# Performance work log

Measured on AMD Instinct MI355X. Metric: run time of the kernel, lower is better.

The kernel has to match this reference:

```python
import jax, jax.numpy as jnp
import numpy as np

B, T = 8, 512
ACT, EMB, DET, HID, NST = 32, 1024, 1024, 1024, 16
STO, CLS = 32, 32
UNIMIX = 0.01


def _ln(x, g, b):
    m = x.mean(-1, keepdims=True)
    v = x.var(-1, keepdims=True)
    return (x - m) / jnp.sqrt(v + 1e-5) * g + b


def _lnsilu(x, g, b):
    return jax.nn.silu(_ln(x, g, b))


def setup_inputs() -> dict:
    key = jax.random.key(0)
    ks = iter(jax.random.split(key, 40))

    def lin(din, dout):
        return jax.random.normal(next(ks), (din, dout), jnp.float32) / np.sqrt(din)

    actions = jax.random.normal(next(ks), (B, T, ACT), jnp.float32)
    embeds = jax.random.normal(next(ks), (B, T, EMB), jnp.float32)
    # pre_ssm: Linear(ACT,HID) + LayerNormSiLU(HID)
    W_pre, b_pre = lin(ACT, HID), jnp.zeros(HID)
    g_pre, bb_pre = jnp.ones(HID), jnp.zeros(HID)
    W_emb = lin(EMB, HID)  # bias=False
    W_in, b_in = lin(HID, 2 * DET), jnp.zeros(2 * DET)
    W_dt = lin(DET, DET)
    # dt bias init: inverse-softplus of dt ~ LogUniform(1e-3, 0.1)
    u = jax.random.uniform(next(ks), (DET,), jnp.float32)
    dt_init = jnp.exp(u * (np.log(0.1) - np.log(1e-3)) + np.log(1e-3))
    b_dt = dt_init + jnp.log(-jnp.expm1(-dt_init))
    W_B, W_C = lin(DET, NST), lin(DET, NST)
    A_log = jnp.broadcast_to(
        jnp.log(jnp.arange(1, NST + 1, dtype=jnp.float32)), (DET, NST)
    ) + jnp.zeros((DET, NST))
    Dp = jnp.ones(DET)
    g_out, b_out = jnp.ones(DET), jnp.zeros(DET)
    # prior_net: Linear(DET,HID)+LNSiLU+Linear(HID,STO*CLS)
    W_pr1, b_pr1 = lin(DET, HID), jnp.zeros(HID)
    g_pr, bb_pr = jnp.ones(HID), jnp.zeros(HID)
    W_pr2, b_pr2 = lin(HID, STO * CLS), jnp.zeros(STO * CLS)
    # post_net: Linear(DET+EMB,HID)+LNSiLU+Linear(HID,STO*CLS)
    W_po1, b_po1 = lin(DET + EMB, HID), jnp.zeros(HID)
    g_po, bb_po = jnp.ones(HID), jnp.zeros(HID)
    W_po2, b_po2 = lin(HID, STO * CLS), jnp.zeros(STO * CLS)
    return dict(actions=actions, embeds=embeds, W_pre=W_pre, b_pre=b_pre,
                g_pre=g_pre, bb_pre=bb_pre, W_emb=W_emb, W_in=W_in, b_in=b_in,
                W_dt=W_dt, b_dt=b_dt, W_B=W_B, W_C=W_C, A_log=A_log, Dp=Dp,
                g_out=g_out, b_out=b_out, W_pr1=W_pr1, b_pr1=b_pr1, g_pr=g_pr,
                bb_pr=bb_pr, W_pr2=W_pr2, b_pr2=b_pr2, W_po1=W_po1, b_po1=b_po1,
                g_po=g_po, bb_po=bb_po, W_po2=W_po2, b_po2=b_po2)


def reference(actions, embeds, W_pre, b_pre, g_pre, bb_pre, W_emb, W_in, b_in,
              W_dt, b_dt, W_B, W_C, A_log, Dp, g_out, b_out, W_pr1, b_pr1,
              g_pr, bb_pr, W_pr2, b_pr2, W_po1, b_po1, g_po, bb_po, W_po2, b_po2):
    # input projections
    x = _lnsilu(actions @ W_pre + b_pre, g_pre, bb_pre) + embeds @ W_emb  # (B,T,HID)
    x = x.transpose(1, 0, 2)  # (T,B,HID)
    xz = x @ W_in + b_in
    x_ssm, x_gate = xz[..., :DET], xz[..., DET:]
    dt = jax.nn.softplus(x_ssm @ W_dt + b_dt)        # (T,B,DET)
    Bp = x_ssm @ W_B                                  # (T,B,NST)
    Cp = x_ssm @ W_C                                  # (T,B,NST)
    A = -jnp.exp(A_log)                               # (DET,NST)
    gates = jnp.exp(dt[..., None] * A)                # (T,B,DET,NST)
    values = (dt * x_ssm)[..., None] * Bp[:, :, None, :]

    # linear recurrence h[t] = g[t]*h[t-1] + v[t] via associative scan
    def comb(a, c):
        g1, v1 = a
        g2, v2 = c
        return (g1 * g2, g2 * v1 + v2)

    _, h = jax.lax.associative_scan(comb, (gates, values), axis=0)
    y = jnp.einsum('tbdn,tbn->tbd', h, Cp) + Dp * x_ssm
    y = y * jax.nn.silu(x_gate)
    deter = _ln(y, g_out, b_out)                      # (T,B,DET)

    # prior / post heads
    prior = _lnsilu(deter @ W_pr1 + b_pr1, g_pr, bb_pr) @ W_pr2 + b_pr2
    emb_t = embeds.transpose(1, 0, 2)
    post_in = jnp.concatenate([deter, emb_t], -1)
    post = _lnsilu(post_in @ W_po1 + b_po1, g_po, bb_po) @ W_po2 + b_po2
    # unimix transform of post logits (deterministic part of _categorical)
    p = jax.nn.softmax(post.reshape(T, B, STO, CLS), -1)
    p = (1.0 - UNIMIX) * p + UNIMIX / CLS
    post_u = jnp.log(p + 1e-8).reshape(T, B, STO * CLS)
    return jnp.concatenate([deter, prior, post_u], -1)  # (T,B,DET+2*STO*CLS)
```

## Files before the change

### kernel.cpp

```cpp
#include <hip/hip_runtime.h>
#include <hip/hip_bf16.h>
#include <math.h>


typedef __bf16 bf16_t;
typedef __bf16 bf16x8 __attribute__((ext_vector_type(8)));
typedef float f32x4 __attribute__((ext_vector_type(4)));

#define B_   8
#define T_   512
#define R_   4096
#define HID_ 1024
#define NC_  32
#define CL_  16

static __device__ __forceinline__ float bf2f(bf16_t x) { return (float)x; }
static __device__ __forceinline__ bf16_t f2bf(float x) { return (bf16_t)x; }
static __device__ __forceinline__ float ldany(const void* p, size_t i, bool isb) {
  return isb ? bf2f(((const bf16_t*)p)[i]) : ((const float*)p)[i];
}

typedef __attribute__((address_space(3))) unsigned int lds_u32;
typedef const __attribute__((address_space(1))) unsigned int glb_u32;
static __device__ __forceinline__ void gld16(const bf16_t* g, bf16_t* l) {
  __builtin_amdgcn_global_load_lds((glb_u32*)g, (lds_u32*)l, 16, 0, 0);
}

__global__ void detect_k(const unsigned int* __restrict__ dp_raw, int* __restrict__ flag) {
  if (threadIdx.x == 0) *flag = (dp_raw[0] == 0x3F803F80u) ? 1 : 0;
}

struct CvtArgs {
  const void* src[17];
  float* dst[17];
  int n[17];
};
__global__ __launch_bounds__(256) void cvt_vecs(CvtArgs a, const int* __restrict__ flag) {
  const bool isb = (*flag != 0);
  int v = blockIdx.y;
  const void* s = a.src[v];
  float* d = a.dst[v];
  int n = a.n[v];
  for (int i = blockIdx.x * 256 + threadIdx.x; i < n; i += 8 * 256)
    d[i] = ldany(s, i, isb);
}

__device__ __forceinline__ void block_sum2(float& s, float& ss) {
#pragma unroll
  for (int off = 32; off > 0; off >>= 1) {
    s  += __shfl_down(s, off, 64);
    ss += __shfl_down(ss, off, 64);
  }
  __shared__ float red[8];
  int tid = threadIdx.x;
  int wave = tid >> 6, lane = tid & 63;
  if (lane == 0) { red[wave] = s; red[4 + wave] = ss; }
  __syncthreads();
  s  = red[0] + red[1] + red[2] + red[3];
  ss = red[4] + red[5] + red[6] + red[7];
}

struct TrArgs {
  const void* src[8];
  bf16_t* dst[8];
  int K[8], N[8];
  int tile0[9];
};
__global__ void tr_batch(TrArgs a, const int* __restrict__ flag) {
  __shared__ float tile[32][33];
  const bool isb = (*flag != 0);
  int bid = blockIdx.x;
  int m = 0;
#pragma unroll
  for (int q = 0; q < 7; ++q) if (bid >= a.tile0[q + 1]) m = q + 1;
  int local = bid - a.tile0[m];
  int K = a.K[m], N = a.N[m];
  int ntx = N >> 5;
  int n0 = (local % ntx) * 32, k0 = (local / ntx) * 32;
  const void* src = a.src[m];
  bf16_t* dst = a.dst[m];
  int tx = threadIdx.x, ty = threadIdx.y;
#pragma unroll
  for (int i = 0; i < 4; ++i) {
    size_t idx = (size_t)(k0 + ty + i * 8) * N + n0 + tx;
    tile[ty + i * 8][tx] = ldany(src, idx, isb);
  }
  __syncthreads();
#pragma unroll
  for (int i = 0; i < 4; ++i)
    dst[(size_t)(n0 + ty + i * 8) * K + k0 + tx] = f2bf(tile[tx][ty + i * 8]);
}

__global__ __launch_bounds__(256) void bc_build(const void* __restrict__ W_B,
                                                const void* __restrict__ W_C,
                                                bf16_t* __restrict__ WTbc,
                                                const int* __restrict__ flag) {
  const bool isb = (*flag != 0);
  int idx = blockIdx.x * 256 + threadIdx.x;
  int r = idx >> 10, k = idx & 1023;
  float v = 0.f;
  if (r < 16)      v = ldany(W_B, k * 16 + r, isb);
  else if (r < 32) v = ldany(W_C, k * 16 + (r - 16), isb);
  WTbc[(size_t)r * 1024 + k] = f2bf(v);
}

__global__ __launch_bounds__(256) void reorder_emb(const void* __restrict__ emb,
                                                   bf16_t* __restrict__ embT,
                                                   const int* __restrict__ flag) {
  const bool isb = (*flag != 0);
  int r = blockIdx.x, tid = threadIdx.x;
  int t = r >> 3, b = r & 7;
  size_t base = (size_t)(b * T_ + t) * 1024;
#pragma unroll
  for (int i = 0; i < 4; ++i) {
    int c = i * 256 + tid;
    embT[(size_t)r * 1024 + c] = f2bf(ldany(emb, base + c, isb));
  }
}

__global__ __launch_bounds__(256) void reorder_act(const void* __restrict__ act,
                                                   bf16_t* __restrict__ actA,
                                                   const int* __restrict__ flag) {
  const bool isb = (*flag != 0);
  int i = blockIdx.x * 256 + threadIdx.x;
  int r = i >> 5, k = i & 31;
  int t = r >> 3, b = r & 7;
  actA[(size_t)r * 32 + k] = f2bf(ldany(act, (size_t)(b * T_ + t) * 32 + k, isb));
}

enum { EPI_ADD_BF16 = 0, EPI_XZ = 1, EPI_SOFTPLUS = 2, EPI_BIAS_F32 = 3,
       EPI_PRIOR = 4, EPI_BC = 5 };

struct GemmArgs {
  const bf16_t* A;
  const bf16_t* Bt;
  int K;
  int N;
  int bnN;
  const float* bias;
  const float* addf;
  float* outf0;
  float* outf1;
  bf16_t* outh0;
  bf16_t* outh1;
  void* outv;
  const int* flag;
};

template <int EPI>
__global__ __launch_bounds__(256) void gemm_t(GemmArgs g) {
  __shared__ __align__(16) bf16_t As[64 * 32];
  __shared__ __align__(16) bf16_t Bs[64 * 32];
  const int tid = threadIdx.x;
  const int wave = tid >> 6, lane = tid & 63;
  const int K = g.K;

  const int per = gridDim.x >> 3;
  const int idx = (blockIdx.x & 7) * per + (blockIdx.x >> 3);
  const int bm = idx / g.bnN, bn = idx % g.bnN;

  f32x4 acc[2][2] = {};

  const int srow = tid >> 2;
  const int scol = (tid & 3) * 8;
  const bf16_t* Ap = g.A  + (size_t)(bm * 64 + srow) * K + scol;
  const bf16_t* Bp = g.Bt + (size_t)(bn * 64 + srow) * K + scol;
  bf16_t* AsW = &As[tid * 8];
  bf16_t* BsW = &Bs[tid * 8];

  const int wm = (wave >> 1) * 32, wn = (wave & 1) * 32;
  const int fm = lane & 15, fk = (lane >> 4) * 8;

  for (int k0 = 0; k0 < K; k0 += 32) {
    gld16(Ap + k0, AsW);
    gld16(Bp + k0, BsW);
    __syncthreads();
    bf16x8 af[2], bfr[2];
#pragma unroll
    for (int i = 0; i < 2; ++i)
      af[i] = *(const bf16x8*)&As[(wm + i * 16 + fm) * 32 + fk];
#pragma unroll
    for (int j = 0; j < 2; ++j)
      bfr[j] = *(const bf16x8*)&Bs[(wn + j * 16 + fm) * 32 + fk];
#pragma unroll
    for (int i = 0; i < 2; ++i)
#pragma unroll
      for (int j = 0; j < 2; ++j)
        acc[i][j] = __builtin_amdgcn_mfma_f32_16x16x32_bf16(af[i], bfr[j], acc[i][j], 0, 0, 0);
    __syncthreads();
  }

  const bool out_bf = (EPI == EPI_PRIOR) ? (*g.flag != 0) : false;
  const int em = (lane >> 4) * 4, en = lane & 15;
#pragma unroll
  for (int i = 0; i < 2; ++i) {
#pragma unroll
    for (int j = 0; j < 2; ++j) {
#pragma unroll
      for (int v = 0; v < 4; ++v) {
        int row = bm * 64 + wm + i * 16 + em + v;
        int col = bn * 64 + wn + j * 16 + en;
        float x = acc[i][j][v];
        if constexpr (EPI == EPI_ADD_BF16) {
          size_t o = (size_t)row * g.N + col;
          g.outh0[o] = f2bf(x + g.addf[o]);
        } else if constexpr (EPI == EPI_XZ) {
          float val = x + g.bias[col];
          if (col < 1024) {
            size_t o = (size_t)row * 1024 + col;
            g.outf0[o] = val;
            g.outh0[o] = f2bf(val);
          } else {
            size_t o = (size_t)row * 1024 + (col - 1024);
            g.outh1[o] = f2bf(val);
          }
        } else if constexpr (EPI == EPI_SOFTPLUS) {
          float val = x + g.bias[col];
          float sp = (val > 20.f) ? val : log1pf(__expf(val));
          g.outf0[(size_t)row * 1024 + col] = sp;
        } else if constexpr (EPI == EPI_BIAS_F32) {
          g.outf0[(size_t)row * g.N + col] = x + g.bias[col];
        } else if constexpr (EPI == EPI_BC) {
          if (col < 16)      g.outf0[(size_t)row * 16 + col] = x;
          else if (col < 32) g.outf1[(size_t)row * 16 + (col - 16)] = x;
        } else {
          float val = x + g.bias[col];
          size_t o = (size_t)row * 3072 + 1024 + col;
          if (out_bf) ((bf16_t*)g.outv)[o] = f2bf(val);
          else        ((float*)g.outv)[o]  = val;
        }
      }
    }
  }
}

__global__ __launch_bounds__(256) void scan_p1(const float* __restrict__ dt,
                                               const float* __restrict__ xs,
                                               const float* __restrict__ Bp,
                                               const float* __restrict__ A_log,
                                               float* __restrict__ Gp,
                                               float* __restrict__ Hl) {
  int idx = blockIdx.x * 256 + threadIdx.x;
  int d = idx & 1023;
  int cb = idx >> 10;
  int b = cb & 7, c = cb >> 3;
  float Ad[16];
#pragma unroll
  for (int n = 0; n < 16; ++n) Ad[n] = -__expf(A_log[d * 16 + n]);
  float h[16] = {};
  float dts = 0.f;
  int r0 = c * CL_ * 8 + b;
  for (int tl = 0; tl < CL_; ++tl) {
    int r = r0 + tl * 8;
    size_t off = (size_t)r * 1024 + d;
    float dtv = dt[off], xv = xs[off];
    float dtx = dtv * xv;
    dts += dtv;
    const float4* Bp4 = (const float4*)(Bp + r * 16);
    float4 b4[4] = {Bp4[0], Bp4[1], Bp4[2], Bp4[3]};
    const float* bv = (const float*)b4;
#pragma unroll
    for (int n = 0; n < 16; ++n) {
      float gg = __expf(dtv * Ad[n]);
      h[n] = gg * h[n] + dtx * bv[n];
    }
  }
  float* gp = Gp + (size_t)idx * 16;
  float* hl = Hl + (size_t)idx * 16;
#pragma unroll
  for (int q = 0; q < 4; ++q) {
    float4 gq, hq;
    gq.x = __expf(dts * Ad[q * 4 + 0]); gq.y = __expf(dts * Ad[q * 4 + 1]);
    gq.z = __expf(dts * Ad[q * 4 + 2]); gq.w = __expf(dts * Ad[q * 4 + 3]);
    hq.x = h[q * 4 + 0]; hq.y = h[q * 4 + 1]; hq.z = h[q * 4 + 2]; hq.w = h[q * 4 + 3];
    ((float4*)gp)[q] = gq;
    ((float4*)hl)[q] = hq;
  }
}

__global__ __launch_bounds__(256) void scan_p2(float* __restrict__ GpCin,
                                               const float* __restrict__ Hl) {
  int j = blockIdx.x * 256 + threadIdx.x;
  float carry = 0.f;
#pragma unroll
  for (int c = 0; c < NC_; ++c) {
    size_t o = (size_t)c * 131072 + j;
    float gv = GpCin[o], hl = Hl[o];
    GpCin[o] = carry;
    carry = gv * carry + hl;
  }
}

__global__ __launch_bounds__(256) void scan_p3(const float* __restrict__ dt,
                                               const float* __restrict__ xs,
                                               const bf16_t* __restrict__ xg,
                                               const float* __restrict__ Bp,
                                               const float* __restrict__ Cp,
                                               const float* __restrict__ A_log,
                                               const float* __restrict__ Dp,
                                               const float* __restrict__ Cin,
                                               float* __restrict__ y) {
  int idx = blockIdx.x * 256 + threadIdx.x;
  int d = idx & 1023;
  int cb = idx >> 10;
  int b = cb & 7, c = cb >> 3;
  float Ad[16];
#pragma unroll
  for (int n = 0; n < 16; ++n) Ad[n] = -__expf(A_log[d * 16 + n]);
  float Dd = Dp[d];
  float h[16];
  const float4* Ci4 = (const float4*)(Cin + (size_t)idx * 16);
#pragma unroll
  for (int q = 0; q < 4; ++q) {
    float4 cq = Ci4[q];
    h[q * 4 + 0] = cq.x; h[q * 4 + 1] = cq.y; h[q * 4 + 2] = cq.z; h[q * 4 + 3] = cq.w;
  }
  int r0 = c * CL_ * 8 + b;
  for (int tl = 0; tl < CL_; ++tl) {
    int r = r0 + tl * 8;
    size_t off = (size_t)r * 1024 + d;
    float dtv = dt[off], xv = xs[off], gv = bf2f(xg[off]);
    float dtx = dtv * xv;
    const float4* Bp4 = (const float4*)(Bp + r * 16);
    const float4* Cp4 = (const float4*)(Cp + r * 16);
    float4 b4[4] = {Bp4[0], Bp4[1], Bp4[2], Bp4[3]};
    float4 c4[4] = {Cp4[0], Cp4[1], Cp4[2], Cp4[3]};
    const float* bv = (const float*)b4;
    const float* cv = (const float*)c4;
    float yv = 0.f;
#pragma unroll
    for (int n = 0; n < 16; ++n) {
      float gg = __expf(dtv * Ad[n]);
      h[n] = gg * h[n] + dtx * bv[n];
      yv += h[n] * cv[n];
    }
    yv += Dd * xv;
    float sg = gv / (1.f + __expf(-gv));
    y[off] = yv * sg;
  }
}

template <int MODE>
__global__ __launch_bounds__(256) void ln_k(const float* __restrict__ in,
                                            const float* __restrict__ gw,
                                            const float* __restrict__ bw,
                                            bf16_t* __restrict__ out0,
                                            void* __restrict__ out1,
                                            float* __restrict__ outf,
                                            const bf16_t* __restrict__ embT,
                                            bf16_t* __restrict__ post_in,
                                            const int* __restrict__ flag) {
  const bool out_bf = (MODE == 0) ? (*flag != 0) : false;
  int r = blockIdx.x, tid = threadIdx.x;
  float v[4];
  float s = 0.f, ss = 0.f;
#pragma unroll
  for (int i = 0; i < 4; ++i) {
    v[i] = in[(size_t)r * 1024 + i * 256 + tid];
    s += v[i]; ss += v[i] * v[i];
  }
  block_sum2(s, ss);
  float mean = s * (1.f / 1024.f);
  float var  = ss * (1.f / 1024.f) - mean * mean;
  float rstd = rsqrtf(var + 1e-5f);
#pragma unroll
  for (int i = 0; i < 4; ++i) {
    int c = i * 256 + tid;
    float yv = (v[i] - mean) * rstd * gw[c] + bw[c];
    if constexpr (MODE >= 1) yv = yv / (1.f + __expf(-yv));
    if constexpr (MODE == 2) {
      outf[(size_t)r * 1024 + c] = yv;
    } else {
      out0[(size_t)r * 1024 + c] = f2bf(yv);
    }
    if constexpr (MODE == 0) {
      size_t o = (size_t)r * 3072 + c;
      if (out_bf) ((bf16_t*)out1)[o] = f2bf(yv);
      else        ((float*)out1)[o]  = yv;
      post_in[(size_t)r * 2048 + c] = f2bf(yv);
      post_in[(size_t)r * 2048 + 1024 + c] = embT[(size_t)r * 1024 + c];
    }
  }
}

__global__ __launch_bounds__(256) void softmax_k(const float* __restrict__ logits,
                                                 void* __restrict__ out,
                                                 const int* __restrict__ flag) {
  const bool out_bf = (*flag != 0);
  int idx = blockIdx.x * 256 + threadIdx.x;
  int r = idx >> 5, grp = idx & 31;
  const float* p = logits + (size_t)r * 1024 + grp * 32;
  float x[32];
  float m = -1e30f;
#pragma unroll
  for (int j = 0; j < 32; ++j) { x[j] = p[j]; m = fmaxf(m, x[j]); }
  float sum = 0.f;
#pragma unroll
  for (int j = 0; j < 32; ++j) { x[j] = __expf(x[j] - m); sum += x[j]; }
  float inv = 0.99f / sum;
  size_t base = (size_t)r * 3072 + 2048 + grp * 32;
#pragma unroll
  for (int j = 0; j < 32; ++j) {
    float val = logf(x[j] * inv + (0.01f / 32.f) + 1e-8f);
    if (out_bf) ((bf16_t*)out)[base + j] = f2bf(val);
    else        ((float*)out)[base + j]  = val;
  }
}

extern "C" void kernel_launch(void* const* d_in, const int* in_sizes, int n_in,
                              void* d_out, int out_size, void* d_ws, size_t ws_size,
                              hipStream_t stream) {
  (void)in_sizes; (void)n_in; (void)out_size; (void)ws_size;
  const void* actions = d_in[0];
  const void* embeds  = d_in[1];
  const void* W_pre   = d_in[2];
  const void* b_pre   = d_in[3];
  const void* g_pre   = d_in[4];
  const void* bb_pre  = d_in[5];
  const void* W_emb   = d_in[6];
  const void* W_in    = d_in[7];
  const void* b_in    = d_in[8];
  const void* W_dt    = d_in[9];
  const void* b_dt    = d_in[10];
  const void* W_B     = d_in[11];
  const void* W_C     = d_in[12];
  const void* A_log   = d_in[13];
  const void* Dp      = d_in[14];
  const void* g_out   = d_in[15];
  const void* b_out   = d_in[16];
  const void* W_pr1   = d_in[17];
  const void* b_pr1   = d_in[18];
  const void* g_pr    = d_in[19];
  const void* bb_pr   = d_in[20];
  const void* W_pr2   = d_in[21];
  const void* b_pr2   = d_in[22];
  const void* W_po1   = d_in[23];
  const void* b_po1   = d_in[24];
  const void* g_po    = d_in[25];
  const void* bb_po   = d_in[26];
  const void* W_po2   = d_in[27];
  const void* b_po2   = d_in[28];

  char* ws = (char*)d_ws;
  const size_t MB = 1ull << 20;
  const size_t KB = 1024;
  bf16_t* WTemb = (bf16_t*)(ws + 0);
  bf16_t* WTin  = (bf16_t*)(ws + 2 * MB);
  bf16_t* WTdt  = (bf16_t*)(ws + 6 * MB);
  bf16_t* WTpr1 = (bf16_t*)(ws + 8 * MB);
  bf16_t* WTpr2 = (bf16_t*)(ws + 10 * MB);
  bf16_t* WTpo1 = (bf16_t*)(ws + 12 * MB);
  bf16_t* WTpo2 = (bf16_t*)(ws + 16 * MB);
  bf16_t* embT  = (bf16_t*)(ws + 18 * MB);
  float*  F1    = (float*)(ws + 26 * MB);
  float*  F2    = (float*)(ws + 42 * MB);
  float*  F5    = (float*)(ws + 58 * MB);
  bf16_t* B8    = (bf16_t*)(ws + 74 * MB);
  bf16_t* B9    = (bf16_t*)(ws + 82 * MB);
  bf16_t* G8    = (bf16_t*)(ws + 90 * MB);
  float*  BpB   = (float*)(ws + 98 * MB);
  float*  CpB   = (float*)(ws + 98 * MB + 256 * KB);
  float*  Hl    = (float*)(ws + 58 * MB);
  float*  Gp    = (float*)(ws + 74 * MB);
  char* cb = ws + 98 * MB + 512 * KB;
  int*   flag    = (int*)(cb);                cb += 256;
  float* Alog_f  = (float*)(cb);              cb += 16384 * 4;
  float* Dp_f    = (float*)(cb);              cb += 1024 * 4;
  float* bpre_f  = (float*)(cb);              cb += 1024 * 4;
  float* gpre_f  = (float*)(cb);              cb += 1024 * 4;
  float* bbpre_f = (float*)(cb);              cb += 1024 * 4;
  float* bin_f   = (float*)(cb);              cb += 2048 * 4;
  float* bdt_f   = (float*)(cb);              cb += 1024 * 4;
  float* gout_f  = (float*)(cb);              cb += 1024 * 4;
  float* bout_f  = (float*)(cb);              cb += 1024 * 4;
  float* bpr1_f  = (float*)(cb);              cb += 1024 * 4;
  float* gpr_f   = (float*)(cb);              cb += 1024 * 4;
  float* bbpr_f  = (float*)(cb);              cb += 1024 * 4;
  float* bpr2_f  = (float*)(cb);              cb += 1024 * 4;
  float* bpo1_f  = (float*)(cb);              cb += 1024 * 4;
  float* gpo_f   = (float*)(cb);              cb += 1024 * 4;
  float* bbpo_f  = (float*)(cb);              cb += 1024 * 4;
  float* bpo2_f  = (float*)(cb);              cb += 1024 * 4;
  bf16_t* WTbc   = (bf16_t*)(cb);             cb += 64 * 1024 * 2;
  bf16_t* actA   = (bf16_t*)(cb);             cb += 4096 * 32 * 2;
  bf16_t* WTpre  = (bf16_t*)(cb);             cb += 1024 * 32 * 2;

  detect_k<<<1, 64, 0, stream>>>((const unsigned int*)Dp, flag);

  CvtArgs ca{};
  const void* srcs[17] = {A_log, Dp, b_pre, g_pre, bb_pre, b_in, b_dt,
                          g_out, b_out, b_pr1, g_pr, bb_pr, b_pr2,
                          b_po1, g_po, bb_po, b_po2};
  float* dsts[17] = {Alog_f, Dp_f, bpre_f, gpre_f, bbpre_f, bin_f, bdt_f,
                     gout_f, bout_f, bpr1_f, gpr_f, bbpr_f, bpr2_f,
                     bpo1_f, gpo_f, bbpo_f, bpo2_f};
  int ns[17] = {16384, 1024, 1024, 1024, 1024, 2048, 1024,
                1024, 1024, 1024, 1024, 1024, 1024,
                1024, 1024, 1024, 1024};
  for (int i = 0; i < 17; ++i) { ca.src[i] = srcs[i]; ca.dst[i] = dsts[i]; ca.n[i] = ns[i]; }
  cvt_vecs<<<dim3(8, 17), 256, 0, stream>>>(ca, flag);

  {
    TrArgs ta{};
    const void* tsrc[8] = {W_emb, W_in, W_dt, W_pr1, W_pr2, W_po1, W_po2, W_pre};
    bf16_t* tdst[8] = {WTemb, WTin, WTdt, WTpr1, WTpr2, WTpo1, WTpo2, WTpre};
    int tK[8] = {1024, 1024, 1024, 1024, 1024, 2048, 1024, 32};
    int tN[8] = {1024, 2048, 1024, 1024, 1024, 1024, 1024, 1024};
    int off = 0;
    for (int i = 0; i < 8; ++i) {
      ta.src[i] = tsrc[i]; ta.dst[i] = tdst[i]; ta.K[i] = tK[i]; ta.N[i] = tN[i];
      ta.tile0[i] = off; off += (tK[i] >> 5) * (tN[i] >> 5);
    }
    ta.tile0[8] = off;
    tr_batch<<<off, dim3(32, 8), 0, stream>>>(ta, flag);
  }
  bc_build<<<256, 256, 0, stream>>>(W_B, W_C, WTbc, flag);

  reorder_emb<<<R_, 256, 0, stream>>>(embeds, embT, flag);
  reorder_act<<<512, 256, 0, stream>>>(actions, actA, flag);

  {
    GemmArgs a{}; a.A = actA; a.Bt = WTpre; a.K = 32; a.N = 1024; a.bnN = 16;
    a.bias = bpre_f; a.outf0 = F5;
    gemm_t<EPI_BIAS_F32><<<1024, 256, 0, stream>>>(a);
  }
  ln_k<2><<<R_, 256, 0, stream>>>(F5, gpre_f, bbpre_f, nullptr, nullptr, F1,
                                  nullptr, nullptr, flag);

  {
    GemmArgs a{}; a.A = embT; a.Bt = WTemb; a.K = 1024; a.N = 1024; a.bnN = 16;
    a.addf = F1; a.outh0 = B8;
    gemm_t<EPI_ADD_BF16><<<1024, 256, 0, stream>>>(a);
  }
  {
    GemmArgs a{}; a.A = B8; a.Bt = WTin; a.K = 1024; a.N = 2048; a.bnN = 32;
    a.bias = bin_f; a.outf0 = F2; a.outh0 = B9; a.outh1 = G8;
    gemm_t<EPI_XZ><<<2048, 256, 0, stream>>>(a);
  }
  {
    GemmArgs a{}; a.A = B9; a.Bt = WTbc; a.K = 1024; a.N = 64; a.bnN = 1;
    a.outf0 = BpB; a.outf1 = CpB;
    gemm_t<EPI_BC><<<64, 256, 0, stream>>>(a);
  }
  {
    GemmArgs a{}; a.A = B9; a.Bt = WTdt; a.K = 1024; a.N = 1024; a.bnN = 16;
    a.bias = bdt_f; a.outf0 = F1;
    gemm_t<EPI_SOFTPLUS><<<1024, 256, 0, stream>>>(a);
  }
  scan_p1<<<1024, 256, 0, stream>>>(F1, F2, BpB, Alog_f, Gp, Hl);
  scan_p2<<<512, 256, 0, stream>>>(Gp, Hl);
  scan_p3<<<1024, 256, 0, stream>>>(F1, F2, G8, BpB, CpB, Alog_f, Dp_f, Gp, F5);
  ln_k<0><<<R_, 256, 0, stream>>>(F5, gout_f, bout_f, B9, d_out, nullptr,
                                  embT, (bf16_t*)F5, flag);
  {
    GemmArgs a{}; a.A = B9; a.Bt = WTpr1; a.K = 1024; a.N = 1024; a.bnN = 16;
    a.bias = bpr1_f; a.outf0 = F1;
    gemm_t<EPI_BIAS_F32><<<1024, 256, 0, stream>>>(a);
  }
  ln_k<1><<<R_, 256, 0, stream>>>(F1, gpr_f, bbpr_f, B8, nullptr, nullptr,
                                  nullptr, nullptr, flag);
  {
    GemmArgs a{}; a.A = B8; a.Bt = WTpr2; a.K = 1024; a.N = 1024; a.bnN = 16;
    a.bias = bpr2_f; a.outv = d_out; a.flag = flag;
    gemm_t<EPI_PRIOR><<<1024, 256, 0, stream>>>(a);
  }
  {
    GemmArgs a{}; a.A = (bf16_t*)F5; a.Bt = WTpo1; a.K = 2048; a.N = 1024; a.bnN = 16;
    a.bias = bpo1_f; a.outf0 = F2;
    gemm_t<EPI_BIAS_F32><<<1024, 256, 0, stream>>>(a);
  }
  ln_k<1><<<R_, 256, 0, stream>>>(F2, gpo_f, bbpo_f, B8, nullptr, nullptr,
                                  nullptr, nullptr, flag);
  {
    GemmArgs a{}; a.A = B8; a.Bt = WTpo2; a.K = 1024; a.N = 1024; a.bnN = 16;
    a.bias = bpo2_f; a.outf0 = F1;
    gemm_t<EPI_BIAS_F32><<<1024, 256, 0, stream>>>(a);
  }
  softmax_k<<<512, 256, 0, stream>>>(F1, d_out, flag);
}
```

Before: 501.2 us.

## Fuse dt and B/C projections into one GEMM, swizzle LDS, shrink intermediates

Concatenates the B/C projection weights after the dt weight so a single GEMM produces the softplus dt plus the Bp/Cp outputs, removing one launch and a second read of the activations. It also XOR-swizzles the LDS tile layout in the GEMM to reduce bank conflicts on fragment loads. The pre-SSM LayerNorm-SiLU output and the x_ssm activation are kept only in bf16 instead of fp32, cutting memory traffic. This trades some precision in the scan inputs for less bandwidth, and it pads the fused N dimension to 1088, which wastes some MFMA work.

```diff
diff --git a/kernel.cpp b/kernel.cpp
--- a/kernel.cpp
+++ b/kernel.cpp
@@ -93,7 +93,7 @@
 
 __global__ __launch_bounds__(256) void bc_build(const void* __restrict__ W_B,
                                                 const void* __restrict__ W_C,
-                                                bf16_t* __restrict__ WTbc,
+                                                bf16_t* __restrict__ WTdtbc,
                                                 const int* __restrict__ flag) {
   const bool isb = (*flag != 0);
   int idx = blockIdx.x * 256 + threadIdx.x;
@@ -101,7 +101,7 @@
   float v = 0.f;
   if (r < 16)      v = ldany(W_B, k * 16 + r, isb);
   else if (r < 32) v = ldany(W_C, k * 16 + (r - 16), isb);
-  WTbc[(size_t)r * 1024 + k] = f2bf(v);
+  WTdtbc[(size_t)(1024 + r) * 1024 + k] = f2bf(v);
 }
 
 __global__ __launch_bounds__(256) void reorder_emb(const void* __restrict__ emb,
@@ -128,8 +128,7 @@
   actA[(size_t)r * 32 + k] = f2bf(ldany(act, (size_t)(b * T_ + t) * 32 + k, isb));
 }
 
-enum { EPI_ADD_BF16 = 0, EPI_XZ = 1, EPI_SOFTPLUS = 2, EPI_BIAS_F32 = 3,
-       EPI_PRIOR = 4, EPI_BC = 5 };
+enum { EPI_ADD_BF16 = 0, EPI_XZ = 1, EPI_BIAS_F32 = 3, EPI_PRIOR = 4, EPI_DTBC = 6 };
 
 struct GemmArgs {
   const bf16_t* A;
@@ -138,9 +137,10 @@
   int N;
   int bnN;
   const float* bias;
-  const float* addf;
+  const bf16_t* addh;
   float* outf0;
   float* outf1;
+  float* outf2;
   bf16_t* outh0;
   bf16_t* outh1;
   void* outv;
@@ -162,14 +162,15 @@
   f32x4 acc[2][2] = {};
 
   const int srow = tid >> 2;
-  const int scol = (tid & 3) * 8;
-  const bf16_t* Ap = g.A  + (size_t)(bm * 64 + srow) * K + scol;
-  const bf16_t* Bp = g.Bt + (size_t)(bn * 64 + srow) * K + scol;
+  const int sblk = (tid & 3) ^ ((srow >> 1) & 3);
+  const bf16_t* Ap = g.A  + (size_t)(bm * 64 + srow) * K + sblk * 8;
+  const bf16_t* Bp = g.Bt + (size_t)(bn * 64 + srow) * K + sblk * 8;
   bf16_t* AsW = &As[tid * 8];
   bf16_t* BsW = &Bs[tid * 8];
 
   const int wm = (wave >> 1) * 32, wn = (wave & 1) * 32;
-  const int fm = lane & 15, fk = (lane >> 4) * 8;
+  const int fm = lane & 15;
+  const int swz = (lane >> 4) ^ ((fm >> 1) & 3);
 
   for (int k0 = 0; k0 < K; k0 += 32) {
     gld16(Ap + k0, AsW);
@@ -178,10 +179,10 @@
     bf16x8 af[2], bfr[2];
 #pragma unroll
     for (int i = 0; i < 2; ++i)
-      af[i] = *(const bf16x8*)&As[(wm + i * 16 + fm) * 32 + fk];
+      af[i] = *(const bf16x8*)&As[((wm + i * 16 + fm) * 4 + swz) * 8];
 #pragma unroll
     for (int j = 0; j < 2; ++j)
-      bfr[j] = *(const bf16x8*)&Bs[(wn + j * 16 + fm) * 32 + fk];
+      bfr[j] = *(const bf16x8*)&Bs[((wn + j * 16 + fm) * 4 + swz) * 8];
 #pragma unroll
     for (int i = 0; i < 2; ++i)
 #pragma unroll
@@ -203,26 +204,23 @@
         float x = acc[i][j][v];
         if constexpr (EPI == EPI_ADD_BF16) {
           size_t o = (size_t)row * g.N + col;
-          g.outh0[o] = f2bf(x + g.addf[o]);
+          g.outh0[o] = f2bf(x + bf2f(g.addh[o]));
         } else if constexpr (EPI == EPI_XZ) {
           float val = x + g.bias[col];
-          if (col < 1024) {
-            size_t o = (size_t)row * 1024 + col;
-            g.outf0[o] = val;
-            g.outh0[o] = f2bf(val);
-          } else {
-            size_t o = (size_t)row * 1024 + (col - 1024);
-            g.outh1[o] = f2bf(val);
-          }
-        } else if constexpr (EPI == EPI_SOFTPLUS) {
-          float val = x + g.bias[col];
-          float sp = (val > 20.f) ? val : log1pf(__expf(val));
-          g.outf0[(size_t)row * 1024 + col] = sp;
+          if (col < 1024) g.outh0[(size_t)row * 1024 + col] = f2bf(val);
+          else            g.outh1[(size_t)row * 1024 + (col - 1024)] = f2bf(val);
         } else if constexpr (EPI == EPI_BIAS_F32) {
           g.outf0[(size_t)row * g.N + col] = x + g.bias[col];
-        } else if constexpr (EPI == EPI_BC) {
-          if (col < 16)      g.outf0[(size_t)row * 16 + col] = x;
-          else if (col < 32) g.outf1[(size_t)row * 16 + (col - 16)] = x;
+        } else if constexpr (EPI == EPI_DTBC) {
+          if (col < 1024) {
+            float val = x + g.bias[col];
+            float sp = (val > 20.f) ? val : log1pf(__expf(val));
+            g.outf0[(size_t)row * 1024 + col] = sp;
+          } else if (col < 1040) {
+            g.outf1[(size_t)row * 16 + (col - 1024)] = x;
+          } else if (col < 1056) {
+            g.outf2[(size_t)row * 16 + (col - 1040)] = x;
+          }
         } else {
           float val = x + g.bias[col];
           size_t o = (size_t)row * 3072 + 1024 + col;
@@ -235,7 +233,7 @@
 }
 
 __global__ __launch_bounds__(256) void scan_p1(const float* __restrict__ dt,
-                                               const float* __restrict__ xs,
+                                               const bf16_t* __restrict__ xsh,
                                                const float* __restrict__ Bp,
                                                const float* __restrict__ A_log,
                                                float* __restrict__ Gp,
@@ -253,7 +251,7 @@
   for (int tl = 0; tl < CL_; ++tl) {
     int r = r0 + tl * 8;
     size_t off = (size_t)r * 1024 + d;
-    float dtv = dt[off], xv = xs[off];
+    float dtv = dt[off], xv = bf2f(xsh[off]);
     float dtx = dtv * xv;
     dts += dtv;
     const float4* Bp4 = (const float4*)(Bp + r * 16);
@@ -292,7 +290,7 @@
 }
 
 __global__ __launch_bounds__(256) void scan_p3(const float* __restrict__ dt,
-                                               const float* __restrict__ xs,
+                                               const bf16_t* __restrict__ xsh,
                                                const bf16_t* __restrict__ xg,
                                                const float* __restrict__ Bp,
                                                const float* __restrict__ Cp,
@@ -319,7 +317,7 @@
   for (int tl = 0; tl < CL_; ++tl) {
     int r = r0 + tl * 8;
     size_t off = (size_t)r * 1024 + d;
-    float dtv = dt[off], xv = xs[off], gv = bf2f(xg[off]);
+    float dtv = dt[off], xv = bf2f(xsh[off]), gv = bf2f(xg[off]);
     float dtx = dtv * xv;
     const float4* Bp4 = (const float4*)(Bp + r * 16);
     const float4* Cp4 = (const float4*)(Cp + r * 16);
@@ -346,7 +344,6 @@
                                             const float* __restrict__ bw,
                                             bf16_t* __restrict__ out0,
                                             void* __restrict__ out1,
-                                            float* __restrict__ outf,
                                             const bf16_t* __restrict__ embT,
                                             bf16_t* __restrict__ post_in,
                                             const int* __restrict__ flag) {
@@ -367,12 +364,8 @@
   for (int i = 0; i < 4; ++i) {
     int c = i * 256 + tid;
     float yv = (v[i] - mean) * rstd * gw[c] + bw[c];
-    if constexpr (MODE >= 1) yv = yv / (1.f + __expf(-yv));
-    if constexpr (MODE == 2) {
-      outf[(size_t)r * 1024 + c] = yv;
-    } else {
-      out0[(size_t)r * 1024 + c] = f2bf(yv);
-    }
+    if constexpr (MODE == 1) yv = yv / (1.f + __expf(-yv));
+    out0[(size_t)r * 1024 + c] = f2bf(yv);
     if constexpr (MODE == 0) {
       size_t o = (size_t)r * 3072 + c;
       if (out_bf) ((bf16_t*)out1)[o] = f2bf(yv);
@@ -442,27 +435,26 @@
   const void* b_po2   = d_in[28];
 
   char* ws = (char*)d_ws;
-  const size_t MB = 1ull << 20;
   const size_t KB = 1024;
-  bf16_t* WTemb = (bf16_t*)(ws + 0);
-  bf16_t* WTin  = (bf16_t*)(ws + 2 * MB);
-  bf16_t* WTdt  = (bf16_t*)(ws + 6 * MB);
-  bf16_t* WTpr1 = (bf16_t*)(ws + 8 * MB);
-  bf16_t* WTpr2 = (bf16_t*)(ws + 10 * MB);
-  bf16_t* WTpo1 = (bf16_t*)(ws + 12 * MB);
-  bf16_t* WTpo2 = (bf16_t*)(ws + 16 * MB);
-  bf16_t* embT  = (bf16_t*)(ws + 18 * MB);
-  float*  F1    = (float*)(ws + 26 * MB);
-  float*  F2    = (float*)(ws + 42 * MB);
-  float*  F5    = (float*)(ws + 58 * MB);
-  bf16_t* B8    = (bf16_t*)(ws + 74 * MB);
-  bf16_t* B9    = (bf16_t*)(ws + 82 * MB);
-  bf16_t* G8    = (bf16_t*)(ws + 90 * MB);
-  float*  BpB   = (float*)(ws + 98 * MB);
-  float*  CpB   = (float*)(ws + 98 * MB + 256 * KB);
-  float*  Hl    = (float*)(ws + 58 * MB);
-  float*  Gp    = (float*)(ws + 74 * MB);
-  char* cb = ws + 98 * MB + 512 * KB;
+  bf16_t* WTemb  = (bf16_t*)(ws + 0 * KB);
+  bf16_t* WTin   = (bf16_t*)(ws + 2048 * KB);
+  bf16_t* WTdtbc = (bf16_t*)(ws + 6144 * KB);
+  bf16_t* WTpr1  = (bf16_t*)(ws + 8320 * KB);
+  bf16_t* WTpr2  = (bf16_t*)(ws + 10368 * KB);
+  bf16_t* WTpo1  = (bf16_t*)(ws + 12416 * KB);
+  bf16_t* WTpo2  = (bf16_t*)(ws + 16512 * KB);
+  bf16_t* embT   = (bf16_t*)(ws + 18560 * KB);
+  float*  F1     = (float*)(ws + 26752 * KB);
+  float*  F2     = (float*)(ws + 43136 * KB);
+  float*  F5     = (float*)(ws + 59520 * KB);
+  bf16_t* B8     = (bf16_t*)(ws + 75904 * KB);
+  bf16_t* B9     = (bf16_t*)(ws + 84096 * KB);
+  bf16_t* G8     = (bf16_t*)(ws + 92288 * KB);
+  float*  BpB    = (float*)(ws + 100480 * KB);
+  float*  CpB    = (float*)(ws + 100736 * KB);
+  float*  Hl     = (float*)(ws + 59520 * KB);
+  float*  Gp     = (float*)(ws + 43136 * KB);
+  char* cb = ws + 100992 * KB;
   int*   flag    = (int*)(cb);                cb += 256;
   float* Alog_f  = (float*)(cb);              cb += 16384 * 4;
   float* Dp_f    = (float*)(cb);              cb += 1024 * 4;
@@ -481,7 +473,6 @@
   float* gpo_f   = (float*)(cb);              cb += 1024 * 4;
   float* bbpo_f  = (float*)(cb);              cb += 1024 * 4;
   float* bpo2_f  = (float*)(cb);              cb += 1024 * 4;
-  bf16_t* WTbc   = (bf16_t*)(cb);             cb += 64 * 1024 * 2;
   bf16_t* actA   = (bf16_t*)(cb);             cb += 4096 * 32 * 2;
   bf16_t* WTpre  = (bf16_t*)(cb);             cb += 1024 * 32 * 2;
 
@@ -503,7 +494,7 @@
   {
     TrArgs ta{};
     const void* tsrc[8] = {W_emb, W_in, W_dt, W_pr1, W_pr2, W_po1, W_po2, W_pre};
-    bf16_t* tdst[8] = {WTemb, WTin, WTdt, WTpr1, WTpr2, WTpo1, WTpo2, WTpre};
+    bf16_t* tdst[8] = {WTemb, WTin, WTdtbc, WTpr1, WTpr2, WTpo1, WTpo2, WTpre};
     int tK[8] = {1024, 1024, 1024, 1024, 1024, 2048, 1024, 32};
     int tN[8] = {1024, 2048, 1024, 1024, 1024, 1024, 1024, 1024};
     int off = 0;
@@ -514,7 +505,7 @@
     ta.tile0[8] = off;
     tr_batch<<<off, dim3(32, 8), 0, stream>>>(ta, flag);
   }
-  bc_build<<<256, 256, 0, stream>>>(W_B, W_C, WTbc, flag);
+  bc_build<<<256, 256, 0, stream>>>(W_B, W_C, WTdtbc, flag);
 
   reorder_emb<<<R_, 256, 0, stream>>>(embeds, embT, flag);
   reorder_act<<<512, 256, 0, stream>>>(actions, actA, flag);
@@ -524,40 +515,34 @@
     a.bias = bpre_f; a.outf0 = F5;
     gemm_t<EPI_BIAS_F32><<<1024, 256, 0, stream>>>(a);
   }
-  ln_k<2><<<R_, 256, 0, stream>>>(F5, gpre_f, bbpre_f, nullptr, nullptr, F1,
+  ln_k<1><<<R_, 256, 0, stream>>>(F5, gpre_f, bbpre_f, B8, nullptr,
                                   nullptr, nullptr, flag);
-
   {
     GemmArgs a{}; a.A = embT; a.Bt = WTemb; a.K = 1024; a.N = 1024; a.bnN = 16;
-    a.addf = F1; a.outh0 = B8;
+    a.addh = B8; a.outh0 = G8;
     gemm_t<EPI_ADD_BF16><<<1024, 256, 0, stream>>>(a);
   }
   {
-    GemmArgs a{}; a.A = B8; a.Bt = WTin; a.K = 1024; a.N = 2048; a.bnN = 32;
-    a.bias = bin_f; a.outf0 = F2; a.outh0 = B9; a.outh1 = G8;
+    GemmArgs a{}; a.A = G8; a.Bt = WTin; a.K = 1024; a.N = 2048; a.bnN = 32;
+    a.bias = bin_f; a.outh0 = B9; a.outh1 = B8;
     gemm_t<EPI_XZ><<<2048, 256, 0, stream>>>(a);
   }
   {
-    GemmArgs a{}; a.A = B9; a.Bt = WTbc; a.K = 1024; a.N = 64; a.bnN = 1;
-    a.outf0 = BpB; a.outf1 = CpB;
-    gemm_t<EPI_BC><<<64, 256, 0, stream>>>(a);
-  }
-  {
-    GemmArgs a{}; a.A = B9; a.Bt = WTdt; a.K = 1024; a.N = 1024; a.bnN = 16;
-    a.bias = bdt_f; a.outf0 = F1;
-    gemm_t<EPI_SOFTPLUS><<<1024, 256, 0, stream>>>(a);
-  }
-  scan_p1<<<1024, 256, 0, stream>>>(F1, F2, BpB, Alog_f, Gp, Hl);
+    GemmArgs a{}; a.A = B9; a.Bt = WTdtbc; a.K = 1024; a.N = 1088; a.bnN = 17;
+    a.bias = bdt_f; a.outf0 = F1; a.outf1 = BpB; a.outf2 = CpB;
+    gemm_t<EPI_DTBC><<<1088, 256, 0, stream>>>(a);
+  }
+  scan_p1<<<1024, 256, 0, stream>>>(F1, B9, BpB, Alog_f, Gp, Hl);
   scan_p2<<<512, 256, 0, stream>>>(Gp, Hl);
-  scan_p3<<<1024, 256, 0, stream>>>(F1, F2, G8, BpB, CpB, Alog_f, Dp_f, Gp, F5);
-  ln_k<0><<<R_, 256, 0, stream>>>(F5, gout_f, bout_f, B9, d_out, nullptr,
+  scan_p3<<<1024, 256, 0, stream>>>(F1, B9, B8, BpB, CpB, Alog_f, Dp_f, Gp, F5);
+  ln_k<0><<<R_, 256, 0, stream>>>(F5, gout_f, bout_f, B9, d_out,
                                   embT, (bf16_t*)F5, flag);
   {
     GemmArgs a{}; a.A = B9; a.Bt = WTpr1; a.K = 1024; a.N = 1024; a.bnN = 16;
     a.bias = bpr1_f; a.outf0 = F1;
     gemm_t<EPI_BIAS_F32><<<1024, 256, 0, stream>>>(a);
   }
-  ln_k<1><<<R_, 256, 0, stream>>>(F1, gpr_f, bbpr_f, B8, nullptr, nullptr,
+  ln_k<1><<<R_, 256, 0, stream>>>(F1, gpr_f, bbpr_f, B8, nullptr,
                                   nullptr, nullptr, flag);
   {
     GemmArgs a{}; a.A = B8; a.Bt = WTpr2; a.K = 1024; a.N = 1024; a.bnN = 16;
@@ -569,7 +554,7 @@
     a.bias = bpo1_f; a.outf0 = F2;
     gemm_t<EPI_BIAS_F32><<<1024, 256, 0, stream>>>(a);
   }
-  ln_k<1><<<R_, 256, 0, stream>>>(F2, gpo_f, bbpo_f, B8, nullptr, nullptr,
+  ln_k<1><<<R_, 256, 0, stream>>>(F2, gpo_f, bbpo_f, B8, nullptr,
                                   nullptr, nullptr, flag);
   {
     GemmArgs a{}; a.A = B8; a.Bt = WTpo2; a.K = 1024; a.N = 1024; a.bnN = 16;
```

New measurement: 479.5 us. -4.3%, faster.
